# Kernel optimization log

Hardware: AMD Instinct MI355X
Metric: run time of the kernel (lower is better)

## Reference

```python
import jax, jax.numpy as jnp
import numpy as np

N, Q, P, S, B = 262144, 256, 10, 8, 4096


def setup_inputs() -> dict:
    key = jax.random.key(0)
    k1, k2, k3, k4 = jax.random.split(key, 4)
    x = jax.random.normal(k1, (N, Q), dtype=jnp.float32)
    beta_u = jax.random.normal(k2, (Q, P, S), dtype=jnp.float32)
    beta_z = jax.random.normal(k3, (Q, P, S), dtype=jnp.float32)
    seg_ids = jnp.sort(jax.random.randint(k4, (N,), 0, B, dtype=jnp.int64))
    return {"x": x, "beta_u": beta_u, "beta_z": beta_z, "seg_ids": seg_ids,
            "num_segments": B}


def reference(x, beta_u, beta_z, seg_ids, num_segments):
    # b = sqrt(mean over feature dim of beta_z^2): [1, P, S]
    b = jnp.sqrt(jnp.mean(beta_z ** 2, axis=0, keepdims=True))
    eta = beta_z / b                                   # [Q, P, S]
    # attention logits per instance: [N, P, S]
    _w = jnp.einsum('iq,qps->ips', x, beta_u)
    # scatter_softmax over instances within each bag (dim 0)
    seg_max = jax.ops.segment_max(_w, seg_ids, num_segments=num_segments)
    ex = jnp.exp(_w - seg_max[seg_ids])
    denom = jax.ops.segment_sum(ex, seg_ids, num_segments=num_segments)
    w = ex / denom[seg_ids]                            # [N, P, S]
    t = jnp.einsum('iq,qps->ips', x, eta)              # [N, P, S]
    # weighted bag pooling (segment_add_csr equivalent): [B, P, S]
    z_bag = jax.ops.segment_sum(w * t, seg_ids, num_segments=num_segments)
    mean = jnp.mean(z_bag, axis=0)
    std = jnp.std(z_bag, axis=0, ddof=1)               # torch .std is unbiased
    std = jnp.where(jnp.isnan(std), jnp.float32(1.0), std)
    return b * (z_bag - mean) / std
```

## Files before the change

kernel.cpp:

```cpp
#include <hip/hip_runtime.h>
#include <hip/hip_bf16.h>
#include <math.h>

#define NN 262144
#define QQ 256
#define PS 80
#define BB 4096
#define NSLOT 4
#define RT 64
#define NITER 8
#define SMEM_BYTES 32768

typedef _Float16 f16x8 __attribute__((ext_vector_type(8)));
typedef float f32x4  __attribute__((ext_vector_type(4)));

__device__ inline unsigned short f16b(float f) {
  return __builtin_bit_cast(unsigned short, (_Float16)f);
}
__device__ inline float f16tof(unsigned short u) {
  return (float)__builtin_bit_cast(_Float16, u);
}

#define LBAR() do {                                                           \
    asm volatile("s_waitcnt lgkmcnt(0)" ::: "memory");                        \
    __builtin_amdgcn_s_barrier();                                             \
    __builtin_amdgcn_sched_barrier(0);                                        \
  } while (0)

__global__ void bprep_k(const float* __restrict__ bu, const float* __restrict__ bz,
                        unsigned short* __restrict__ bFlat) {
  int gid = blockIdx.x * 256 + threadIdx.x;
  if (gid >= 5120) return;
  int kt  = gid / 640;
  int rem = gid - kt * 640;
  int kg  = rem / 160;
  int c   = rem - kg * 160;
  unsigned short* dst = bFlat + (size_t)gid * 8;
  int kbase = kt * 32 + kg * 8;
#pragma unroll
  for (int j = 0; j < 8; ++j) {
    int k = kbase + j;
    float v = (c < PS) ? bu[k * PS + c] : bz[k * PS + (c - PS)];
    dst[j] = f16b(v);
  }
}

__global__ void seg_bounds_k(const int* __restrict__ seg, int* __restrict__ segstart) {
  int b = blockIdx.x * blockDim.x + threadIdx.x;
  if (b > BB) return;
  if (b == BB) { segstart[BB] = NN; return; }
  int lo = 0, hi = NN;
  while (lo < hi) {
    int mid = (lo + hi) >> 1;
    if (seg[mid] < b) lo = mid + 1; else hi = mid;
  }
  segstart[b] = lo;
}

__global__ __launch_bounds__(256, 4) void fused_k(
    const float* __restrict__ x, const unsigned short* __restrict__ bFlat,
    const int* __restrict__ seg, const int* __restrict__ segstart,
    float* __restrict__ pm, float* __restrict__ pse, float* __restrict__ pst) {
  __shared__ __align__(16) char smem[SMEM_BYTES];
  const int tid  = threadIdx.x;
  const int lane = tid & 63;
  const int wid  = tid >> 6;
  const int rs   = blockIdx.x * RT;

  const int wr   = (wid & 1) * 32;
  const int cw   = wid >> 1;
  const int lrow = lane & 15;
  const int lk16 = lane >> 4;

  const int ra = tid >> 2;
  const int kg = tid & 3;
  const float* xp = x + (size_t)(rs + ra) * QQ + kg * 8;
  char* adst = smem + kg * 1024 + ((ra ^ (kg << 2)) * 16);

  const unsigned short* bA = bFlat + ((size_t)lk16 * 160 + cw * 80 + lrow) * 8;
  const int aoff0 = lk16 * 1024 + (((wr + lrow)      ^ (lk16 << 2)) * 16);
  const int aoff1 = lk16 * 1024 + (((wr + 16 + lrow) ^ (lk16 << 2)) * 16);

  f16x8 br[2][5];
#define LOADB(s_, t_) do {                                                    \
    _Pragma("unroll")                                                         \
    for (int n_ = 0; n_ < 5; ++n_)                                            \
      br[s_][n_] = *reinterpret_cast<const f16x8*>(bA + (t_) * 5120 + n_ * 128); \
  } while (0)

#define WRITEA(kt_) do {                                                      \
    float4 v0 = xs[2 * (kt_)], v1 = xs[2 * (kt_) + 1];                        \
    unsigned short a0 = f16b(v0.x), a1 = f16b(v0.y), a2 = f16b(v0.z), a3 = f16b(v0.w); \
    unsigned short a4 = f16b(v1.x), a5 = f16b(v1.y), a6 = f16b(v1.z), a7 = f16b(v1.w); \
    uint4 w = make_uint4((unsigned)a0 | ((unsigned)a1 << 16),                 \
                         (unsigned)a2 | ((unsigned)a3 << 16),                 \
                         (unsigned)a4 | ((unsigned)a5 << 16),                 \
                         (unsigned)a6 | ((unsigned)a7 << 16));                \
    *reinterpret_cast<uint4*>(adst + (kt_) * 4096) = w;                       \
  } while (0)

#define KITER(t_) do {                                                        \
    const int s_ = (t_) & 1;                                                  \
    f16x8 a0 = *reinterpret_cast<const f16x8*>(smem + (t_) * 4096 + aoff0);   \
    f16x8 a1 = *reinterpret_cast<const f16x8*>(smem + (t_) * 4096 + aoff1);   \
    __builtin_amdgcn_s_setprio(1);                                            \
    _Pragma("unroll")                                                         \
    for (int n_ = 0; n_ < 5; ++n_) {                                          \
      acc[0][n_] = __builtin_amdgcn_mfma_f32_16x16x32_f16(a0, br[s_][n_], acc[0][n_], 0, 0, 0); \
      acc[1][n_] = __builtin_amdgcn_mfma_f32_16x16x32_f16(a1, br[s_][n_], acc[1][n_], 0, 0, 0); \
    }                                                                         \
    __builtin_amdgcn_s_setprio(0);                                            \
    if ((t_) < NITER - 2) LOADB(s_, (t_) + 2);                                \
  } while (0)

  float4 xs[16];
#pragma unroll
  for (int kt = 0; kt < NITER; ++kt) {
    xs[2 * kt]     = *reinterpret_cast<const float4*>(xp + kt * 32);
    xs[2 * kt + 1] = *reinterpret_cast<const float4*>(xp + kt * 32 + 4);
  }
  LOADB(0, 0);
  LOADB(1, 1);

  f32x4 acc[2][5];
#pragma unroll
  for (int m = 0; m < 2; ++m)
#pragma unroll
    for (int n = 0; n < 5; ++n) acc[m][n] = (f32x4){0.f, 0.f, 0.f, 0.f};

#pragma unroll
  for (int kt = 0; kt < 4; ++kt) WRITEA(kt);
  LBAR();

  KITER(0); KITER(1); KITER(2); KITER(3);

#pragma unroll
  for (int kt = 4; kt < 8; ++kt) WRITEA(kt);
  LBAR();

  KITER(4); KITER(5); KITER(6); KITER(7);
#undef LOADB
#undef WRITEA
#undef KITER

  __syncthreads();
  float* res_u          = reinterpret_cast<float*>(smem);
  unsigned short* res_v = reinterpret_cast<unsigned short*>(smem + 20480);
#pragma unroll
  for (int m = 0; m < 2; ++m)
#pragma unroll
    for (int n = 0; n < 5; ++n)
#pragma unroll
      for (int rr = 0; rr < 4; ++rr) {
        int row = wr + m * 16 + lk16 * 4 + rr;
        int col = n * 16 + lrow;
        if (cw == 0) res_u[row * 80 + col] = acc[m][n][rr];
        else         res_v[row * 80 + col] = f16b(acc[m][n][rr]);
      }
  __syncthreads();

  int b0 = seg[rs];
  int b1 = seg[rs + RT - 1];
  int nu = (b1 - b0 + 1) * PS;
  for (int u = tid; u < nu; u += 256) {
    int bag = b0 + u / PS;
    int c   = u % PS;
    int sb  = segstart[bag];
    int lo  = max(sb, rs) - rs;
    int hi  = min(segstart[bag + 1], rs + RT) - rs;
    float m_ = -3.4e38f, se = 0.f, st = 0.f;
    for (int r = lo; r < hi; ++r) {
      float v  = res_u[r * 80 + c];
      float tv = f16tof(res_v[r * 80 + c]);
      float nm = fmaxf(m_, v);
      float sc = __expf(m_ - nm);
      float ee = __expf(v - nm);
      se = se * sc + ee;
      st = st * sc + ee * tv;
      m_ = nm;
    }
    int slot = blockIdx.x - (sb >> 6);
    size_t p = ((size_t)bag * NSLOT + slot) * PS + c;
    pm[p] = m_; pse[p] = se; pst[p] = st;
  }
}

__device__ inline float wave_sum(float v) {
#pragma unroll
  for (int o = 32; o > 0; o >>= 1) v += __shfl_down(v, o, 64);
  return v;
}

__global__ __launch_bounds__(256) void combfin_k(
    const int* __restrict__ segstart,
    const float* __restrict__ pm, const float* __restrict__ pse,
    const float* __restrict__ pst, const float* __restrict__ bz,
    float* __restrict__ out) {
  const int c = blockIdx.x;
  const int t = threadIdx.x;
  __shared__ float zsh[BB];

  float bvz = bz[t * PS + c];
  float bsq = bvz * bvz;

  float s = 0.f, ss = 0.f;
  for (int b = t; b < BB; b += 256) {
    int sb = segstart[b], eb = segstart[b + 1];
    float z = 0.f;
    if (eb > sb) {
      int ns = ((eb - 1) >> 6) - (sb >> 6) + 1;
      ns = min(ns, NSLOT);
      float m = -3.4e38f, se = 0.f, st = 0.f;
      for (int sl = 0; sl < ns; ++sl) {
        size_t p = ((size_t)b * NSLOT + sl) * PS + c;
        float m2 = pm[p], se2 = pse[p], st2 = pst[p];
        float nm = fmaxf(m, m2);
        float s1 = __expf(m - nm);
        float s2 = __expf(m2 - nm);
        se = se * s1 + se2 * s2;
        st = st * s1 + st2 * s2;
        m = nm;
      }
      z = st / se;
    }
    zsh[b] = z;
    s += z;
    ss += z * z;
  }

  __shared__ float w0[4], w1[4], w2[4];
  float a0 = wave_sum(bsq);
  float a1 = wave_sum(s);
  float a2 = wave_sum(ss);
  int wid = t >> 6, lane = t & 63;
  if (lane == 0) { w0[wid] = a0; w1[wid] = a1; w2[wid] = a2; }
  __syncthreads();

  __shared__ float sh[3];
  if (t == 0) {
    float B0 = w0[0] + w0[1] + w0[2] + w0[3];
    float S1 = w1[0] + w1[1] + w1[2] + w1[3];
    float S2 = w2[0] + w2[1] + w2[2] + w2[3];
    float bval = sqrtf(B0 / (float)QQ);
    float mean = S1 / (float)BB;
    float var = (S2 - (float)BB * mean * mean) / (float)(BB - 1);
    float sd = sqrtf(fmaxf(var, 0.f));
    if (!(sd > 0.f) || sd != sd) sd = 1.f;
    sh[0] = bval; sh[1] = mean; sh[2] = sd;
  }
  __syncthreads();
  float bval = sh[0], mean = sh[1], sd = sh[2];
  for (int b = t; b < BB; b += 256) {
    out[b * PS + c] = bval * (zsh[b] - mean) / sd;
  }
}

extern "C" void kernel_launch(void* const* d_in, const int* in_sizes, int n_in,
                              void* d_out, int out_size, void* d_ws, size_t ws_size,
                              hipStream_t stream) {
  const float* x   = (const float*)d_in[0];
  const float* bu  = (const float*)d_in[1];
  const float* bz  = (const float*)d_in[2];
  const int*   seg = (const int*)d_in[3];
  float* out = (float*)d_out;

  char* ws = (char*)d_ws;
  int* segstart         = (int*)ws;
  unsigned short* bFlat = (unsigned short*)(ws + 16640);
  size_t pn  = (size_t)BB * NSLOT * PS;
  float* pm  = (float*)(ws + 98560);
  float* pse = pm + pn;
  float* pst = pse + pn;

  bprep_k<<<20, 256, 0, stream>>>(bu, bz, bFlat);
  seg_bounds_k<<<(BB + 1 + 255) / 256, 256, 0, stream>>>(seg, segstart);
  fused_k<<<NN / RT, 256, 0, stream>>>(x, bFlat, seg, segstart, pm, pse, pst);
  combfin_k<<<PS, 256, 0, stream>>>(segstart, pm, pse, pst, bz, out);
}
```

Baseline: 118.7 us.

## Stream x loads in quarters and merge prep kernels into one launch

The two small preprocessing kernels (B-matrix fp16 packing and segment-boundary binary search) are combined into a single launch, which removes one kernel launch and its gap. In the fused GEMM kernel, the 16 float4 x prefetch registers are replaced by a double-buffered 8-register quarter pipeline, and B fragments drop from double to single buffering. This cuts register pressure, which may allow more occupancy. The cost is more LDS barriers (four instead of two) and less latency hiding for the B loads.

```diff
diff --git a/kernel.cpp b/kernel.cpp
--- a/kernel.cpp
+++ b/kernel.cpp
@@ -27,34 +27,33 @@
     __builtin_amdgcn_sched_barrier(0);                                        \
   } while (0)
 
-__global__ void bprep_k(const float* __restrict__ bu, const float* __restrict__ bz,
-                        unsigned short* __restrict__ bFlat) {
-  int gid = blockIdx.x * 256 + threadIdx.x;
-  if (gid >= 5120) return;
-  int kt  = gid / 640;
-  int rem = gid - kt * 640;
-  int kg  = rem / 160;
-  int c   = rem - kg * 160;
-  unsigned short* dst = bFlat + (size_t)gid * 8;
-  int kbase = kt * 32 + kg * 8;
-#pragma unroll
-  for (int j = 0; j < 8; ++j) {
-    int k = kbase + j;
-    float v = (c < PS) ? bu[k * PS + c] : bz[k * PS + (c - PS)];
-    dst[j] = f16b(v);
-  }
-}
-
-__global__ void seg_bounds_k(const int* __restrict__ seg, int* __restrict__ segstart) {
-  int b = blockIdx.x * blockDim.x + threadIdx.x;
-  if (b > BB) return;
-  if (b == BB) { segstart[BB] = NN; return; }
-  int lo = 0, hi = NN;
-  while (lo < hi) {
-    int mid = (lo + hi) >> 1;
-    if (seg[mid] < b) lo = mid + 1; else hi = mid;
-  }
-  segstart[b] = lo;
+__global__ void prep_k(const float* __restrict__ bu, const float* __restrict__ bz,
+                       unsigned short* __restrict__ bFlat,
+                       const int* __restrict__ seg, int* __restrict__ segstart) {
+  int g = blockIdx.x * 256 + threadIdx.x;
+  if (g < 5120) {
+    int kt  = g / 640;
+    int rem = g - kt * 640;
+    int kg  = rem / 160;
+    int c   = rem - kg * 160;
+    unsigned short* dst = bFlat + (size_t)g * 8;
+    int kbase = kt * 32 + kg * 8;
+#pragma unroll
+    for (int j = 0; j < 8; ++j) {
+      int k = kbase + j;
+      float v = (c < PS) ? bu[k * PS + c] : bz[k * PS + (c - PS)];
+      dst[j] = f16b(v);
+    }
+  } else if (g <= 5120 + BB) {
+    int b = g - 5120;
+    if (b == BB) { segstart[BB] = NN; return; }
+    int lo = 0, hi = NN;
+    while (lo < hi) {
+      int mid = (lo + hi) >> 1;
+      if (seg[mid] < b) lo = mid + 1; else hi = mid;
+    }
+    segstart[b] = lo;
+  }
 }
 
 __global__ __launch_bounds__(256, 4) void fused_k(
@@ -81,46 +80,48 @@
   const int aoff0 = lk16 * 1024 + (((wr + lrow)      ^ (lk16 << 2)) * 16);
   const int aoff1 = lk16 * 1024 + (((wr + 16 + lrow) ^ (lk16 << 2)) * 16);
 
-  f16x8 br[2][5];
-#define LOADB(s_, t_) do {                                                    \
+  float4 xq[2][4];
+  f16x8  br[5];
+
+#define LOADQ(q_) do {                                                        \
+    xq[(q_) & 1][0] = *reinterpret_cast<const float4*>(xp + (2*(q_))  *32);   \
+    xq[(q_) & 1][1] = *reinterpret_cast<const float4*>(xp + (2*(q_))  *32+4); \
+    xq[(q_) & 1][2] = *reinterpret_cast<const float4*>(xp + (2*(q_)+1)*32);   \
+    xq[(q_) & 1][3] = *reinterpret_cast<const float4*>(xp + (2*(q_)+1)*32+4); \
+  } while (0)
+
+#define LOADB(t_) do {                                                        \
     _Pragma("unroll")                                                         \
     for (int n_ = 0; n_ < 5; ++n_)                                            \
-      br[s_][n_] = *reinterpret_cast<const f16x8*>(bA + (t_) * 5120 + n_ * 128); \
-  } while (0)
-
-#define WRITEA(kt_) do {                                                      \
-    float4 v0 = xs[2 * (kt_)], v1 = xs[2 * (kt_) + 1];                        \
-    unsigned short a0 = f16b(v0.x), a1 = f16b(v0.y), a2 = f16b(v0.z), a3 = f16b(v0.w); \
-    unsigned short a4 = f16b(v1.x), a5 = f16b(v1.y), a6 = f16b(v1.z), a7 = f16b(v1.w); \
-    uint4 w = make_uint4((unsigned)a0 | ((unsigned)a1 << 16),                 \
-                         (unsigned)a2 | ((unsigned)a3 << 16),                 \
-                         (unsigned)a4 | ((unsigned)a5 << 16),                 \
-                         (unsigned)a6 | ((unsigned)a7 << 16));                \
-    *reinterpret_cast<uint4*>(adst + (kt_) * 4096) = w;                       \
+      br[n_] = *reinterpret_cast<const f16x8*>(bA + (t_) * 5120 + n_ * 128);  \
+  } while (0)
+
+#define WRITEQ(q_) do {                                                       \
+    _Pragma("unroll")                                                         \
+    for (int kk_ = 0; kk_ < 2; ++kk_) {                                       \
+      float4 v0 = xq[(q_) & 1][2 * kk_], v1 = xq[(q_) & 1][2 * kk_ + 1];      \
+      unsigned short a0 = f16b(v0.x), a1 = f16b(v0.y), a2 = f16b(v0.z), a3 = f16b(v0.w); \
+      unsigned short a4 = f16b(v1.x), a5 = f16b(v1.y), a6 = f16b(v1.z), a7 = f16b(v1.w); \
+      uint4 w = make_uint4((unsigned)a0 | ((unsigned)a1 << 16),               \
+                           (unsigned)a2 | ((unsigned)a3 << 16),               \
+                           (unsigned)a4 | ((unsigned)a5 << 16),               \
+                           (unsigned)a6 | ((unsigned)a7 << 16));              \
+      *reinterpret_cast<uint4*>(adst + (2 * (q_) + kk_) * 4096) = w;          \
+    }                                                                         \
   } while (0)
 
 #define KITER(t_) do {                                                        \
-    const int s_ = (t_) & 1;                                                  \
     f16x8 a0 = *reinterpret_cast<const f16x8*>(smem + (t_) * 4096 + aoff0);   \
     f16x8 a1 = *reinterpret_cast<const f16x8*>(smem + (t_) * 4096 + aoff1);   \
     __builtin_amdgcn_s_setprio(1);                                            \
     _Pragma("unroll")                                                         \
     for (int n_ = 0; n_ < 5; ++n_) {                                          \
-      acc[0][n_] = __builtin_amdgcn_mfma_f32_16x16x32_f16(a0, br[s_][n_], acc[0][n_], 0, 0, 0); \
-      acc[1][n_] = __builtin_amdgcn_mfma_f32_16x16x32_f16(a1, br[s_][n_], acc[1][n_], 0, 0, 0); \
+      acc[0][n_] = __builtin_amdgcn_mfma_f32_16x16x32_f16(a0, br[n_], acc[0][n_], 0, 0, 0); \
+      acc[1][n_] = __builtin_amdgcn_mfma_f32_16x16x32_f16(a1, br[n_], acc[1][n_], 0, 0, 0); \
     }                                                                         \
     __builtin_amdgcn_s_setprio(0);                                            \
-    if ((t_) < NITER - 2) LOADB(s_, (t_) + 2);                                \
-  } while (0)
-
-  float4 xs[16];
-#pragma unroll
-  for (int kt = 0; kt < NITER; ++kt) {
-    xs[2 * kt]     = *reinterpret_cast<const float4*>(xp + kt * 32);
-    xs[2 * kt + 1] = *reinterpret_cast<const float4*>(xp + kt * 32 + 4);
-  }
-  LOADB(0, 0);
-  LOADB(1, 1);
+    if ((t_) < NITER - 1) LOADB((t_) + 1);                                    \
+  } while (0)
 
   f32x4 acc[2][5];
 #pragma unroll
@@ -128,19 +129,34 @@
 #pragma unroll
     for (int n = 0; n < 5; ++n) acc[m][n] = (f32x4){0.f, 0.f, 0.f, 0.f};
 
-#pragma unroll
-  for (int kt = 0; kt < 4; ++kt) WRITEA(kt);
-  LBAR();
-
-  KITER(0); KITER(1); KITER(2); KITER(3);
-
-#pragma unroll
-  for (int kt = 4; kt < 8; ++kt) WRITEA(kt);
-  LBAR();
-
-  KITER(4); KITER(5); KITER(6); KITER(7);
+  LOADQ(0);
+  LOADQ(1);
+  LOADB(0);
+
+  WRITEQ(0);
+  LBAR();
+  KITER(0);
+  LOADQ(2);
+  KITER(1);
+
+  WRITEQ(1);
+  LBAR();
+  KITER(2);
+  LOADQ(3);
+  KITER(3);
+
+  WRITEQ(2);
+  LBAR();
+  KITER(4);
+  KITER(5);
+
+  WRITEQ(3);
+  LBAR();
+  KITER(6);
+  KITER(7);
+#undef LOADQ
 #undef LOADB
-#undef WRITEA
+#undef WRITEQ
 #undef KITER
 
   __syncthreads();
@@ -272,8 +288,7 @@
   float* pse = pm + pn;
   float* pst = pse + pn;
 
-  bprep_k<<<20, 256, 0, stream>>>(bu, bz, bFlat);
-  seg_bounds_k<<<(BB + 1 + 255) / 256, 256, 0, stream>>>(seg, segstart);
+  prep_k<<<(5120 + BB + 1 + 255) / 256, 256, 0, stream>>>(bu, bz, bFlat, seg, segstart);
   fused_k<<<NN / RT, 256, 0, stream>>>(x, bFlat, seg, segstart, pm, pse, pst);
   combfin_k<<<PS, 256, 0, stream>>>(segstart, pm, pse, pst, bz, out);
 }
```

New measurement: 122.7 us. +3.4%, slower.

## Stream x tiles directly into LDS via global_load_lds and merge prep kernels

Applied to the files above, without the earlier changes.

Replaces the register-staged load of x (fp32 load, convert to f16, write LDS) with direct global-to-LDS async loads of fp32 data into an XOR-swizzled 64KB buffer. Each k-step then waits on a specific vmcnt and converts to f16 when reading its A fragment, so later tiles keep loading while earlier ones are computed. Doubling LDS cuts occupancy to 2 blocks per CU (launch bounds lowered to 2). The two small prep kernels are also fused into one launch to save launch overhead.

```diff
diff --git a/kernel.cpp b/kernel.cpp
--- a/kernel.cpp
+++ b/kernel.cpp
@@ -9,10 +9,12 @@
 #define NSLOT 4
 #define RT 64
 #define NITER 8
-#define SMEM_BYTES 32768
+#define SMEM_BYTES 65536
 
 typedef _Float16 f16x8 __attribute__((ext_vector_type(8)));
 typedef float f32x4  __attribute__((ext_vector_type(4)));
+typedef const __attribute__((address_space(1))) unsigned int g_u32;
+typedef __attribute__((address_space(3))) unsigned int l_u32;
 
 __device__ inline unsigned short f16b(float f) {
   return __builtin_bit_cast(unsigned short, (_Float16)f);
@@ -21,43 +23,36 @@
   return (float)__builtin_bit_cast(_Float16, u);
 }
 
-#define LBAR() do {                                                           \
-    asm volatile("s_waitcnt lgkmcnt(0)" ::: "memory");                        \
-    __builtin_amdgcn_s_barrier();                                             \
-    __builtin_amdgcn_sched_barrier(0);                                        \
-  } while (0)
-
-__global__ void bprep_k(const float* __restrict__ bu, const float* __restrict__ bz,
-                        unsigned short* __restrict__ bFlat) {
-  int gid = blockIdx.x * 256 + threadIdx.x;
-  if (gid >= 5120) return;
-  int kt  = gid / 640;
-  int rem = gid - kt * 640;
-  int kg  = rem / 160;
-  int c   = rem - kg * 160;
-  unsigned short* dst = bFlat + (size_t)gid * 8;
-  int kbase = kt * 32 + kg * 8;
-#pragma unroll
-  for (int j = 0; j < 8; ++j) {
-    int k = kbase + j;
-    float v = (c < PS) ? bu[k * PS + c] : bz[k * PS + (c - PS)];
-    dst[j] = f16b(v);
-  }
-}
-
-__global__ void seg_bounds_k(const int* __restrict__ seg, int* __restrict__ segstart) {
-  int b = blockIdx.x * blockDim.x + threadIdx.x;
-  if (b > BB) return;
-  if (b == BB) { segstart[BB] = NN; return; }
-  int lo = 0, hi = NN;
-  while (lo < hi) {
-    int mid = (lo + hi) >> 1;
-    if (seg[mid] < b) lo = mid + 1; else hi = mid;
-  }
-  segstart[b] = lo;
-}
-
-__global__ __launch_bounds__(256, 4) void fused_k(
+__global__ void prep_k(const float* __restrict__ bu, const float* __restrict__ bz,
+                       unsigned short* __restrict__ bFlat,
+                       const int* __restrict__ seg, int* __restrict__ segstart) {
+  int g = blockIdx.x * 256 + threadIdx.x;
+  if (g < 5120) {
+    int kt  = g / 640;
+    int rem = g - kt * 640;
+    int kg  = rem / 160;
+    int c   = rem - kg * 160;
+    unsigned short* dst = bFlat + (size_t)g * 8;
+    int kbase = kt * 32 + kg * 8;
+#pragma unroll
+    for (int j = 0; j < 8; ++j) {
+      int k = kbase + j;
+      float v = (c < PS) ? bu[k * PS + c] : bz[k * PS + (c - PS)];
+      dst[j] = f16b(v);
+    }
+  } else if (g <= 5120 + BB) {
+    int b = g - 5120;
+    if (b == BB) { segstart[BB] = NN; return; }
+    int lo = 0, hi = NN;
+    while (lo < hi) {
+      int mid = (lo + hi) >> 1;
+      if (seg[mid] < b) lo = mid + 1; else hi = mid;
+    }
+    segstart[b] = lo;
+  }
+}
+
+__global__ __launch_bounds__(256, 2) void fused_k(
     const float* __restrict__ x, const unsigned short* __restrict__ bFlat,
     const int* __restrict__ seg, const int* __restrict__ segstart,
     float* __restrict__ pm, float* __restrict__ pse, float* __restrict__ pst) {
@@ -72,76 +67,70 @@
   const int lrow = lane & 15;
   const int lk16 = lane >> 4;
 
-  const int ra = tid >> 2;
-  const int kg = tid & 3;
-  const float* xp = x + (size_t)(rs + ra) * QQ + kg * 8;
-  char* adst = smem + kg * 1024 + ((ra ^ (kg << 2)) * 16);
+  const int l8 = lane >> 3;
+  const int g8 = (lane & 7) ^ l8;
+  const int w8a = wid * 2, w8b = wid * 2 + 1;
+  const float* srcA = x + (size_t)(rs + w8a * 8 + l8) * QQ + g8 * 4;
+  const float* srcB = x + (size_t)(rs + w8b * 8 + l8) * QQ + g8 * 4;
+  char* dstA = smem + w8a * 1024;
+  char* dstB = smem + w8b * 1024;
+#pragma unroll
+  for (int kt = 0; kt < NITER; ++kt) {
+    __builtin_amdgcn_global_load_lds((g_u32*)(srcA + kt * 32),
+                                     (l_u32*)(dstA + kt * 8192), 16, 0, 0);
+    __builtin_amdgcn_global_load_lds((g_u32*)(srcB + kt * 32),
+                                     (l_u32*)(dstB + kt * 8192), 16, 0, 0);
+  }
+  asm volatile("" ::: "memory");
 
   const unsigned short* bA = bFlat + ((size_t)lk16 * 160 + cw * 80 + lrow) * 8;
-  const int aoff0 = lk16 * 1024 + (((wr + lrow)      ^ (lk16 << 2)) * 16);
-  const int aoff1 = lk16 * 1024 + (((wr + 16 + lrow) ^ (lk16 << 2)) * 16);
-
   f16x8 br[2][5];
 #define LOADB(s_, t_) do {                                                    \
     _Pragma("unroll")                                                         \
     for (int n_ = 0; n_ < 5; ++n_)                                            \
       br[s_][n_] = *reinterpret_cast<const f16x8*>(bA + (t_) * 5120 + n_ * 128); \
   } while (0)
-
-#define WRITEA(kt_) do {                                                      \
-    float4 v0 = xs[2 * (kt_)], v1 = xs[2 * (kt_) + 1];                        \
-    unsigned short a0 = f16b(v0.x), a1 = f16b(v0.y), a2 = f16b(v0.z), a3 = f16b(v0.w); \
-    unsigned short a4 = f16b(v1.x), a5 = f16b(v1.y), a6 = f16b(v1.z), a7 = f16b(v1.w); \
-    uint4 w = make_uint4((unsigned)a0 | ((unsigned)a1 << 16),                 \
-                         (unsigned)a2 | ((unsigned)a3 << 16),                 \
-                         (unsigned)a4 | ((unsigned)a5 << 16),                 \
-                         (unsigned)a6 | ((unsigned)a7 << 16));                \
-    *reinterpret_cast<uint4*>(adst + (kt_) * 4096) = w;                       \
-  } while (0)
-
-#define KITER(t_) do {                                                        \
+  LOADB(0, 0);
+  LOADB(1, 1);
+  asm volatile("" ::: "memory");
+
+  f32x4 acc[2][5];
+#pragma unroll
+  for (int m = 0; m < 2; ++m)
+#pragma unroll
+    for (int n = 0; n < 5; ++n) acc[m][n] = (f32x4){0.f, 0.f, 0.f, 0.f};
+
+#define KITER(t_, v_) do {                                                    \
+    asm volatile("s_waitcnt vmcnt(" #v_ ")" ::: "memory");                    \
+    __builtin_amdgcn_s_barrier();                                             \
     const int s_ = (t_) & 1;                                                  \
-    f16x8 a0 = *reinterpret_cast<const f16x8*>(smem + (t_) * 4096 + aoff0);   \
-    f16x8 a1 = *reinterpret_cast<const f16x8*>(smem + (t_) * 4096 + aoff1);   \
+    f16x8 af[2];                                                              \
+    _Pragma("unroll")                                                         \
+    for (int m_ = 0; m_ < 2; ++m_) {                                          \
+      int r_ = wr + m_ * 16 + lrow;                                           \
+      int s0_ = (2 * lk16) ^ (r_ & 7);                                        \
+      const char* base_ = smem + (t_) * 8192 + (r_ >> 3) * 1024 + (r_ & 7) * 128; \
+      f32x4 c0 = *reinterpret_cast<const f32x4*>(base_ + s0_ * 16);           \
+      f32x4 c1 = *reinterpret_cast<const f32x4*>(base_ + (s0_ ^ 1) * 16);     \
+      af[m_][0] = (_Float16)c0[0]; af[m_][1] = (_Float16)c0[1];               \
+      af[m_][2] = (_Float16)c0[2]; af[m_][3] = (_Float16)c0[3];               \
+      af[m_][4] = (_Float16)c1[0]; af[m_][5] = (_Float16)c1[1];               \
+      af[m_][6] = (_Float16)c1[2]; af[m_][7] = (_Float16)c1[3];               \
+    }                                                                         \
     __builtin_amdgcn_s_setprio(1);                                            \
     _Pragma("unroll")                                                         \
     for (int n_ = 0; n_ < 5; ++n_) {                                          \
-      acc[0][n_] = __builtin_amdgcn_mfma_f32_16x16x32_f16(a0, br[s_][n_], acc[0][n_], 0, 0, 0); \
-      acc[1][n_] = __builtin_amdgcn_mfma_f32_16x16x32_f16(a1, br[s_][n_], acc[1][n_], 0, 0, 0); \
+      acc[0][n_] = __builtin_amdgcn_mfma_f32_16x16x32_f16(af[0], br[s_][n_], acc[0][n_], 0, 0, 0); \
+      acc[1][n_] = __builtin_amdgcn_mfma_f32_16x16x32_f16(af[1], br[s_][n_], acc[1][n_], 0, 0, 0); \
     }                                                                         \
     __builtin_amdgcn_s_setprio(0);                                            \
     if ((t_) < NITER - 2) LOADB(s_, (t_) + 2);                                \
   } while (0)
 
-  float4 xs[16];
-#pragma unroll
-  for (int kt = 0; kt < NITER; ++kt) {
-    xs[2 * kt]     = *reinterpret_cast<const float4*>(xp + kt * 32);
-    xs[2 * kt + 1] = *reinterpret_cast<const float4*>(xp + kt * 32 + 4);
-  }
-  LOADB(0, 0);
-  LOADB(1, 1);
-
-  f32x4 acc[2][5];
-#pragma unroll
-  for (int m = 0; m < 2; ++m)
-#pragma unroll
-    for (int n = 0; n < 5; ++n) acc[m][n] = (f32x4){0.f, 0.f, 0.f, 0.f};
-
-#pragma unroll
-  for (int kt = 0; kt < 4; ++kt) WRITEA(kt);
-  LBAR();
-
-  KITER(0); KITER(1); KITER(2); KITER(3);
-
-#pragma unroll
-  for (int kt = 4; kt < 8; ++kt) WRITEA(kt);
-  LBAR();
-
-  KITER(4); KITER(5); KITER(6); KITER(7);
+  KITER(0, 24); KITER(1, 27); KITER(2, 30); KITER(3, 33);
+  KITER(4, 36); KITER(5, 39); KITER(6, 42); KITER(7, 45);
+#undef KITER
 #undef LOADB
-#undef WRITEA
-#undef KITER
 
   __syncthreads();
   float* res_u          = reinterpret_cast<float*>(smem);
@@ -272,8 +261,7 @@
   float* pse = pm + pn;
   float* pst = pse + pn;
 
-  bprep_k<<<20, 256, 0, stream>>>(bu, bz, bFlat);
-  seg_bounds_k<<<(BB + 1 + 255) / 256, 256, 0, stream>>>(seg, segstart);
+  prep_k<<<(5120 + BB + 1 + 255) / 256, 256, 0, stream>>>(bu, bz, bFlat, seg, segstart);
   fused_k<<<NN / RT, 256, 0, stream>>>(x, bFlat, seg, segstart, pm, pse, pst);
   combfin_k<<<PS, 256, 0, stream>>>(segstart, pm, pse, pst, bz, out);
 }
```

After: 144.3 us. 1.22x slower.
